# Optimization experiments

Measured on AMD Instinct MI355X. Metric: run time of the kernel, lower is better.

The kernel has to match this reference:

```python
import math
import jax, jax.numpy as jnp
import numpy as np

WINDOW_SHAPE = [30, 30, 8]
DEPTH = 8
NUM_DIMS = 3
N_POINTS = 2_000_000
BATCH = 4
SPARSE_SHAPE = np.array([32, 512, 512], dtype=np.int64)  # [D, H, W]


def _right_shift_bits(b, k):
    # shift bit-array right along last axis: prepend k zeros, drop last k
    if b.shape[-1] <= k:
        return jnp.zeros_like(b)
    pad = [(0, 0)] * (b.ndim - 1) + [(k, 0)]
    return jnp.pad(b[..., :-k], pad)


def _gray2binary(gray):
    # prefix-XOR along last axis via doubling (matches torch gray2binary)
    n = gray.shape[-1]
    shift = 2 ** (math.ceil(math.log2(n)) - 1)
    while shift > 0:
        gray = jnp.logical_xor(gray, _right_shift_bits(gray, shift))
        shift //= 2
    return gray


def hilbert_encode(locs, num_dims, num_bits):
    # locs: [N, num_dims] int, each in [0, 2**num_bits)
    n = locs.shape[0]
    # bit b of gray is the (num_bits-1-b)-th bit of the coordinate (MSB first)
    shifts_ = (num_bits - 1 - jnp.arange(num_bits, dtype=locs.dtype))
    gray = ((locs[:, :, None] >> shifts_[None, None, :]) & 1).astype(bool)  # [N, D, B]
    # Skilling's transform: small fixed loop (num_bits*num_dims = 24 iters)
    for bit in range(num_bits):
        for dim in range(num_dims):
            mask = gray[:, dim, bit]  # [N]
            g0 = jnp.logical_xor(gray[:, 0, bit + 1:], mask[:, None])
            gray = gray.at[:, 0, bit + 1:].set(g0)
            to_flip = jnp.logical_and(
                jnp.logical_not(mask)[:, None],
                jnp.logical_xor(gray[:, 0, bit + 1:], gray[:, dim, bit + 1:]),
            )
            gray = gray.at[:, dim, bit + 1:].set(
                jnp.logical_xor(gray[:, dim, bit + 1:], to_flip))
            gray = gray.at[:, 0, bit + 1:].set(
                jnp.logical_xor(gray[:, 0, bit + 1:], to_flip))
    # interleave: swapaxes(1,2) then flatten -> [N, num_bits*num_dims], MSB first
    bits = jnp.transpose(gray, (0, 2, 1)).reshape(n, num_bits * num_dims)
    hb = _gray2binary(bits)
    nb = num_bits * num_dims
    weights = jnp.asarray((1 << (nb - 1 - np.arange(nb))), dtype=jnp.int32)
    code = (hb.astype(jnp.int32) * weights).sum(-1)
    return code


def setup_inputs() -> dict:
    key = jax.random.key(0)
    kb, kz, ky, kx = jax.random.split(key, 4)
    D, H, W = [int(v) for v in SPARSE_SHAPE]
    b = jax.random.randint(kb, (N_POINTS,), 0, BATCH, dtype=jnp.int32)
    z = jax.random.randint(kz, (N_POINTS,), 0, D, dtype=jnp.int32)
    y = jax.random.randint(ky, (N_POINTS,), 0, H, dtype=jnp.int32)
    x = jax.random.randint(kx, (N_POINTS,), 0, W, dtype=jnp.int32)
    coords = jnp.stack([b, z, y, x], axis=-1)  # [N, 4]: bs, z, y, x
    return {"coords": coords, "sparse_shape": SPARSE_SHAPE, "shifts": 1}


def reference(coords, sparse_shape, shifts):
    # sparse_shape is static config: [D, H, W]; reversed -> W, H, D (as in torch)
    ss = [int(v) for v in np.asarray(sparse_shape)][::-1]
    W, H, D = ss
    wx, wy, wz = WINDOW_SHAPE
    if bool(shifts):
        sx, sy, sz = math.ceil(wx / 2), math.ceil(wy / 2), math.ceil(wz / 2)
    else:
        sx = sy = sz = 0
    b = coords[:, 0]
    x = (coords[:, 3] + sx) % W
    y = (coords[:, 2] + sy) % H
    z = (coords[:, 1] + sz) % D
    locs = jnp.stack([x, y, z], axis=-1)  # [N, 3]
    code = hilbert_encode(locs, NUM_DIMS, DEPTH)
    code = code | (b.astype(code.dtype) << (DEPTH * 3))
    coords2curve = jnp.argsort(code)
    return coords2curve
```

## Files before the change

### kernel.cpp

```cpp
#include <hip/hip_runtime.h>
#include <stdint.h>


#define THREADS 512
#define TILE 4096
#define ROUNDS (TILE / THREADS)
#define WAVES (THREADS / 64)
#define CHUNK (TILE / WAVES)
#define IDX_BITS 22
#define IDX_MASK 0x3FFFFFu

__device__ __forceinline__ int tile_of(int bid, int nwg) {
  int q = nwg >> 3, r = nwg & 7;
  int x = bid & 7, k = bid >> 3;
  return x * q + (x < r ? x : r) + k;
}

__device__ __forceinline__ uint32_t hilbert_code(uint32_t x, uint32_t y, uint32_t z) {
  uint32_t X0 = x & 255u, X1 = y & 255u, X2 = z & 255u;
#pragma unroll
  for (int p = 7; p >= 0; --p) {
    uint32_t low = (1u << p) - 1u;
    uint32_t f0 = (uint32_t)-(int)((X0 >> p) & 1u);
    X0 ^= (low & f0);
    uint32_t f1 = (uint32_t)-(int)((X1 >> p) & 1u);
    uint32_t t1 = ((X0 ^ X1) & low) & ~f1;
    X0 ^= (low & f1) ^ t1;
    X1 ^= t1;
    uint32_t f2 = (uint32_t)-(int)((X2 >> p) & 1u);
    uint32_t t2 = ((X0 ^ X2) & low) & ~f2;
    X0 ^= (low & f2) ^ t2;
    X2 ^= t2;
  }
  uint32_t G = 0;
#pragma unroll
  for (int k = 0; k < 8; ++k) {
    int p = 7 - k;
    G |= ((X0 >> p) & 1u) << (23 - 3 * k);
    G |= ((X1 >> p) & 1u) << (22 - 3 * k);
    G |= ((X2 >> p) & 1u) << (21 - 3 * k);
  }
  G ^= G >> 16; G ^= G >> 8; G ^= G >> 4; G ^= G >> 2; G ^= G >> 1;
  return G & 0xFFFFFFu;
}

__global__ __launch_bounds__(THREADS) void genkeys_hist(
    const int4* __restrict__ coords, const void* __restrict__ ss,
    const int* __restrict__ shifts, uint32_t* __restrict__ keys0,
    int* __restrict__ hist, int N) {
  __shared__ int lh[512];
  int t = threadIdx.x, b = tile_of(blockIdx.x, gridDim.x);
  lh[t] = 0;

  const int* p32 = (const int*)ss;
  int D, H, W;
  if (p32[1] == 0) { const long long* p64 = (const long long*)ss;
    D = (int)p64[0]; H = (int)p64[1]; W = (int)p64[2]; }
  else { D = p32[0]; H = p32[1]; W = p32[2]; }
  int sflag = shifts[0];
  int sx = sflag ? 15 : 0, sy = sflag ? 15 : 0, sz = sflag ? 4 : 0;
  bool wp2 = (W & (W - 1)) == 0, hp2 = (H & (H - 1)) == 0, dp2 = (D & (D - 1)) == 0;
  __syncthreads();

#pragma unroll
  for (int r = 0; r < ROUNDS; ++r) {
    int idx = b * TILE + r * THREADS + t;
    if (idx < N) {
      int4 c = coords[idx];
      uint32_t bb = (uint32_t)c.x;
      int zz = c.y + sz, yy = c.z + sy, xx = c.w + sx;
      uint32_t z = (uint32_t)(dp2 ? (zz & (D - 1)) : (zz % D));
      uint32_t y = (uint32_t)(hp2 ? (yy & (H - 1)) : (yy % H));
      uint32_t x = (uint32_t)(wp2 ? (xx & (W - 1)) : (xx % W));
      uint32_t code = hilbert_code(x, y, z) | (bb << 24);
      keys0[idx] = code;
      atomicAdd(&lh[code & 511u], 1);
    }
  }
  __syncthreads();
  hist[(size_t)b * 512 + t] = lh[t];
}

template <int SHIFT, int NB>
__global__ __launch_bounds__(THREADS) void hist_kernel(
    const uint32_t* __restrict__ keys, int* __restrict__ hist, int N) {
  __shared__ int lh[NB];
  int t = threadIdx.x, b = tile_of(blockIdx.x, gridDim.x);
  if (t < NB) lh[t] = 0;
  __syncthreads();
#pragma unroll
  for (int r = 0; r < ROUNDS; ++r) {
    int idx = b * TILE + r * THREADS + t;
    if (idx < N) atomicAdd(&lh[(keys[idx] >> SHIFT) & (NB - 1)], 1);
  }
  __syncthreads();
  if (t < NB) hist[(size_t)b * NB + t] = lh[t];
}

__global__ __launch_bounds__(512) void scan_blocks(
    int* __restrict__ hist, int* __restrict__ digitTotals, int nblocks, int nbins) {
  __shared__ int wsum[8];
  int d = blockIdx.x, t = threadIdx.x, wave = t >> 6, lane = t & 63;
  int carry = 0;
  for (int start = 0; start < nblocks; start += 512) {
    int i = start + t;
    int vv = (i < nblocks) ? hist[(size_t)i * nbins + d] : 0;
    int x = vv;
#pragma unroll
    for (int off = 1; off < 64; off <<= 1) {
      int n = __shfl_up(x, off);
      if (lane >= off) x += n;
    }
    if (lane == 63) wsum[wave] = x;
    __syncthreads();
    int pre = 0;
    for (int w = 0; w < wave; ++w) pre += wsum[w];
    if (i < nblocks) hist[(size_t)i * nbins + d] = carry + pre + x - vv;
    int tot = 0;
    for (int w = 0; w < 8; ++w) tot += wsum[w];
    __syncthreads();
    carry += tot;
  }
  if (t == 0) digitTotals[d] = carry;
}

template <int MODE>
__global__ __launch_bounds__(THREADS) void scatter_kernel(
    const uint32_t* __restrict__ in0, const uint32_t* __restrict__ in1,
    uint32_t* __restrict__ out0, uint32_t* __restrict__ out1,
    const int* __restrict__ hist, const int* __restrict__ digitTotals, int N) {
  constexpr int NB = (MODE == 2) ? 256 : 512;
  constexpr int RB = (MODE == 2) ? 8 : 9;
  constexpr int SHIFT = (MODE == 0) ? 0 : (MODE == 1) ? 9 : 22;
  __shared__ uint64_t sbuf[(MODE == 2) ? TILE / 2 : TILE];
  __shared__ __align__(16) unsigned short cnt[WAVES][NB];
  int t = threadIdx.x, b = tile_of(blockIdx.x, gridDim.x);
  int wave = t >> 6, lane = t & 63;

  int histv = 0, dt = 0;
  if (t < NB) {
    histv = hist[(size_t)b * NB + t];
    dt = digitTotals[t];
  }
  for (int i = t; i < WAVES * NB; i += THREADS) ((unsigned short*)cnt)[i] = 0;
  __syncthreads();

  uint64_t kvR[ROUNDS];
  int drR[ROUNDS];
  uint64_t ltm = (1ull << lane) - 1ull;
  int chunk0 = b * TILE + wave * CHUNK;

#pragma unroll
  for (int r = 0; r < ROUNDS; ++r) {
    int idx = chunk0 + r * 64 + lane;
    bool valid = idx < N;
    uint32_t a = valid ? in0[idx] : 0u;
    uint64_t kv;
    if (MODE == 0)      kv = ((uint64_t)(uint32_t)idx << 32) | a;
    else if (MODE == 1) kv = ((uint64_t)(valid ? in1[idx] : 0u) << 32) | a;
    else                kv = a;
    kvR[r] = kv;
    int digit = (int)((a >> SHIFT) & (NB - 1));
    uint64_t eq = __ballot(valid);
#pragma unroll
    for (int bit = 0; bit < RB; ++bit) {
      uint64_t m = __ballot((digit >> bit) & 1);
      eq &= ((digit >> bit) & 1) ? m : ~m;
    }
    int waveRank = __popcll(eq & ltm);
    int cntW = __popcll(eq);
    int prior = cnt[wave][digit];
    drR[r] = valid ? (digit | ((prior + waveRank) << RB)) : -1;
    if (valid && waveRank == 0) cnt[wave][digit] = (unsigned short)(prior + cntW);
  }
  __syncthreads();

  int2* wt = (int2*)sbuf;
  int tot = 0, adjv = 0;
  int2 v = make_int2(0, 0);
  if (t < NB) {
#pragma unroll
    for (int w = 0; w < WAVES; ++w) tot += cnt[w][t];
    v = make_int2(tot, dt);
#pragma unroll
    for (int off = 1; off < 64; off <<= 1) {
      int nx = __shfl_up(v.x, off), ny = __shfl_up(v.y, off);
      if (lane >= off) { v.x += nx; v.y += ny; }
    }
    if (lane == 63) wt[wave] = v;
  }
  __syncthreads();
  if (t < NB) {
    int2 pre = make_int2(0, 0);
    for (int w = 0; w < wave; ++w) { pre.x += wt[w].x; pre.y += wt[w].y; }
    int ds = pre.x + v.x - tot;
    adjv = histv + (pre.y + v.y - dt) - ds;
    int run = ds;
#pragma unroll
    for (int w = 0; w < WAVES; ++w) {
      int x = cnt[w][t];
      cnt[w][t] = (unsigned short)run;
      run += x;
    }
  }
  __syncthreads();

#pragma unroll
  for (int r = 0; r < ROUNDS; ++r) {
    int dr = drR[r];
    if (dr >= 0) {
      int digit = dr & (NB - 1);
      int rnk = dr >> RB;
      int slot = (int)cnt[wave][digit] + rnk;
      if (MODE == 2) ((uint32_t*)sbuf)[slot] = (uint32_t)kvR[r];
      else           sbuf[slot] = kvR[r];
    }
  }
  __syncthreads();

  int* adjArr = (int*)cnt;
  if (t < NB) adjArr[t] = adjv;
  __syncthreads();

  int validCount = min(TILE, N - b * TILE);
#pragma unroll
  for (int j = 0; j < ROUNDS; ++j) {
    int i = j * THREADS + t;
    if (i < validCount) {
      if (MODE == 0) {
        uint64_t kv = sbuf[i];
        uint32_t key = (uint32_t)kv;
        int pos = adjArr[key & 511u] + i;
        out0[pos] = key;
        out1[pos] = (uint32_t)(kv >> 32);
      } else if (MODE == 1) {
        uint64_t kv = sbuf[i];
        uint32_t key = (uint32_t)kv, idxv = (uint32_t)(kv >> 32);
        int pos = adjArr[(key >> 9) & 511u] + i;
        out0[pos] = ((key >> 18) << IDX_BITS) | idxv;
      } else {
        uint32_t p = ((uint32_t*)sbuf)[i];
        int pos = adjArr[(p >> IDX_BITS) & 255u] + i;
        out0[pos] = p & IDX_MASK;
      }
    }
  }
}

extern "C" void kernel_launch(void* const* d_in, const int* in_sizes, int n_in,
                              void* d_out, int out_size, void* d_ws, size_t ws_size,
                              hipStream_t stream) {
  const int4* coords = (const int4*)d_in[0];
  const void* ss = d_in[1];
  const int* shifts = (const int*)d_in[2];
  int N = in_sizes[0] / 4;
  int nblocks = (N + TILE - 1) / TILE;

  char* ws = (char*)d_ws;
  size_t off = 0;
  auto alloc = [&](size_t bytes) -> void* {
    void* p = ws + off;
    off += (bytes + 255) & ~(size_t)255;
    return p;
  };
  uint32_t* keys0 = (uint32_t*)alloc((size_t)N * 4);
  uint32_t* keys1 = (uint32_t*)alloc((size_t)N * 4);
  uint32_t* vals1 = (uint32_t*)alloc((size_t)N * 4);
  uint32_t* packd = (uint32_t*)alloc((size_t)N * 4);
  int*      hist  = (int*)alloc((size_t)512 * nblocks * 4);
  int*      digitTotals = (int*)alloc(512 * 4);

  genkeys_hist<<<nblocks, THREADS, 0, stream>>>(coords, ss, shifts, keys0, hist, N);
  scan_blocks<<<512, 512, 0, stream>>>(hist, digitTotals, nblocks, 512);
  scatter_kernel<0><<<nblocks, THREADS, 0, stream>>>(
      keys0, nullptr, keys1, vals1, hist, digitTotals, N);

  hist_kernel<9, 512><<<nblocks, THREADS, 0, stream>>>(keys1, hist, N);
  scan_blocks<<<512, 512, 0, stream>>>(hist, digitTotals, nblocks, 512);
  scatter_kernel<1><<<nblocks, THREADS, 0, stream>>>(
      keys1, vals1, packd, nullptr, hist, digitTotals, N);

  hist_kernel<22, 256><<<nblocks, THREADS, 0, stream>>>(packd, hist, N);
  scan_blocks<<<256, 512, 0, stream>>>(hist, digitTotals, nblocks, 256);
  scatter_kernel<2><<<nblocks, THREADS, 0, stream>>>(
      packd, nullptr, (uint32_t*)d_out, nullptr, hist, digitTotals, N);
}
```

Measured before the change: 82.60 us.

## Fuse next-pass histograms into radix scatter and double last-pass tile size

Removes the two standalone histogram kernels. Each scatter pass now accumulates the next pass's per-tile digit histogram with global atomics, keyed by output position. This saves a full read of the keys per pass and two launches, at the cost of up to one global atomic per element and a memset of the histogram buffers. The final 8-bit pass now uses 8192-element tiles, halving its block count and doubling per-thread register and LDS footprint.

```diff
diff --git a/kernel.cpp b/kernel.cpp
--- a/kernel.cpp
+++ b/kernel.cpp
@@ -4,9 +4,9 @@
 
 #define THREADS 512
 #define TILE 4096
+#define TILE2 8192
 #define ROUNDS (TILE / THREADS)
 #define WAVES (THREADS / 64)
-#define CHUNK (TILE / WAVES)
 #define IDX_BITS 22
 #define IDX_MASK 0x3FFFFFu
 
@@ -81,22 +81,6 @@
   hist[(size_t)b * 512 + t] = lh[t];
 }
 
-template <int SHIFT, int NB>
-__global__ __launch_bounds__(THREADS) void hist_kernel(
-    const uint32_t* __restrict__ keys, int* __restrict__ hist, int N) {
-  __shared__ int lh[NB];
-  int t = threadIdx.x, b = tile_of(blockIdx.x, gridDim.x);
-  if (t < NB) lh[t] = 0;
-  __syncthreads();
-#pragma unroll
-  for (int r = 0; r < ROUNDS; ++r) {
-    int idx = b * TILE + r * THREADS + t;
-    if (idx < N) atomicAdd(&lh[(keys[idx] >> SHIFT) & (NB - 1)], 1);
-  }
-  __syncthreads();
-  if (t < NB) hist[(size_t)b * NB + t] = lh[t];
-}
-
 __global__ __launch_bounds__(512) void scan_blocks(
     int* __restrict__ hist, int* __restrict__ digitTotals, int nblocks, int nbins) {
   __shared__ int wsum[8];
@@ -128,11 +112,15 @@
 __global__ __launch_bounds__(THREADS) void scatter_kernel(
     const uint32_t* __restrict__ in0, const uint32_t* __restrict__ in1,
     uint32_t* __restrict__ out0, uint32_t* __restrict__ out1,
-    const int* __restrict__ hist, const int* __restrict__ digitTotals, int N) {
+    const int* __restrict__ hist, const int* __restrict__ digitTotals,
+    int* __restrict__ histNext, int N) {
   constexpr int NB = (MODE == 2) ? 256 : 512;
   constexpr int RB = (MODE == 2) ? 8 : 9;
   constexpr int SHIFT = (MODE == 0) ? 0 : (MODE == 1) ? 9 : 22;
-  __shared__ uint64_t sbuf[(MODE == 2) ? TILE / 2 : TILE];
+  constexpr int TB = (MODE == 2) ? TILE2 : TILE;
+  constexpr int RNDS = TB / THREADS;
+  constexpr int CH = TB / WAVES;
+  __shared__ uint64_t sbuf[(MODE == 2) ? TILE2 / 2 : TILE];
   __shared__ __align__(16) unsigned short cnt[WAVES][NB];
   int t = threadIdx.x, b = tile_of(blockIdx.x, gridDim.x);
   int wave = t >> 6, lane = t & 63;
@@ -145,13 +133,13 @@
   for (int i = t; i < WAVES * NB; i += THREADS) ((unsigned short*)cnt)[i] = 0;
   __syncthreads();
 
-  uint64_t kvR[ROUNDS];
-  int drR[ROUNDS];
+  uint64_t kvR[RNDS];
+  int drR[RNDS];
   uint64_t ltm = (1ull << lane) - 1ull;
-  int chunk0 = b * TILE + wave * CHUNK;
-
-#pragma unroll
-  for (int r = 0; r < ROUNDS; ++r) {
+  int chunk0 = b * TB + wave * CH;
+
+#pragma unroll
+  for (int r = 0; r < RNDS; ++r) {
     int idx = chunk0 + r * 64 + lane;
     bool valid = idx < N;
     uint32_t a = valid ? in0[idx] : 0u;
@@ -206,7 +194,7 @@
   __syncthreads();
 
 #pragma unroll
-  for (int r = 0; r < ROUNDS; ++r) {
+  for (int r = 0; r < RNDS; ++r) {
     int dr = drR[r];
     if (dr >= 0) {
       int digit = dr & (NB - 1);
@@ -222,9 +210,9 @@
   if (t < NB) adjArr[t] = adjv;
   __syncthreads();
 
-  int validCount = min(TILE, N - b * TILE);
-#pragma unroll
-  for (int j = 0; j < ROUNDS; ++j) {
+  int validCount = min(TB, N - b * TB);
+#pragma unroll
+  for (int j = 0; j < RNDS; ++j) {
     int i = j * THREADS + t;
     if (i < validCount) {
       if (MODE == 0) {
@@ -233,11 +221,13 @@
         int pos = adjArr[key & 511u] + i;
         out0[pos] = key;
         out1[pos] = (uint32_t)(kv >> 32);
+        atomicAdd(&histNext[(size_t)(pos >> 12) * 512 + ((key >> 9) & 511u)], 1);
       } else if (MODE == 1) {
         uint64_t kv = sbuf[i];
         uint32_t key = (uint32_t)kv, idxv = (uint32_t)(kv >> 32);
         int pos = adjArr[(key >> 9) & 511u] + i;
         out0[pos] = ((key >> 18) << IDX_BITS) | idxv;
+        atomicAdd(&histNext[(size_t)(pos >> 13) * 256 + ((key >> 18) & 255u)], 1);
       } else {
         uint32_t p = ((uint32_t*)sbuf)[i];
         int pos = adjArr[(p >> IDX_BITS) & 255u] + i;
@@ -255,6 +245,7 @@
   const int* shifts = (const int*)d_in[2];
   int N = in_sizes[0] / 4;
   int nblocks = (N + TILE - 1) / TILE;
+  int nblocks2 = (N + TILE2 - 1) / TILE2;
 
   char* ws = (char*)d_ws;
   size_t off = 0;
@@ -267,21 +258,24 @@
   uint32_t* keys1 = (uint32_t*)alloc((size_t)N * 4);
   uint32_t* vals1 = (uint32_t*)alloc((size_t)N * 4);
   uint32_t* packd = (uint32_t*)alloc((size_t)N * 4);
-  int*      hist  = (int*)alloc((size_t)512 * nblocks * 4);
+  int*      histA = (int*)alloc((size_t)512 * nblocks * 4);
+  int*      histB = (int*)alloc((size_t)512 * nblocks * 4);
+  int*      histC = (int*)alloc((size_t)256 * nblocks2 * 4);
   int*      digitTotals = (int*)alloc(512 * 4);
 
-  genkeys_hist<<<nblocks, THREADS, 0, stream>>>(coords, ss, shifts, keys0, hist, N);
-  scan_blocks<<<512, 512, 0, stream>>>(hist, digitTotals, nblocks, 512);
+  size_t zbytes = (size_t)((char*)histC - (char*)histB) + (size_t)256 * nblocks2 * 4;
+  hipMemsetAsync(histB, 0, zbytes, stream);
+
+  genkeys_hist<<<nblocks, THREADS, 0, stream>>>(coords, ss, shifts, keys0, histA, N);
+  scan_blocks<<<512, 512, 0, stream>>>(histA, digitTotals, nblocks, 512);
   scatter_kernel<0><<<nblocks, THREADS, 0, stream>>>(
-      keys0, nullptr, keys1, vals1, hist, digitTotals, N);
-
-  hist_kernel<9, 512><<<nblocks, THREADS, 0, stream>>>(keys1, hist, N);
-  scan_blocks<<<512, 512, 0, stream>>>(hist, digitTotals, nblocks, 512);
+      keys0, nullptr, keys1, vals1, histA, digitTotals, histB, N);
+
+  scan_blocks<<<512, 512, 0, stream>>>(histB, digitTotals, nblocks, 512);
   scatter_kernel<1><<<nblocks, THREADS, 0, stream>>>(
-      keys1, vals1, packd, nullptr, hist, digitTotals, N);
-
-  hist_kernel<22, 256><<<nblocks, THREADS, 0, stream>>>(packd, hist, N);
-  scan_blocks<<<256, 512, 0, stream>>>(hist, digitTotals, nblocks, 256);
-  scatter_kernel<2><<<nblocks, THREADS, 0, stream>>>(
-      packd, nullptr, (uint32_t*)d_out, nullptr, hist, digitTotals, N);
-}
+      keys1, vals1, packd, nullptr, histB, digitTotals, histC, N);
+
+  scan_blocks<<<256, 512, 0, stream>>>(histC, digitTotals, nblocks2, 256);
+  scatter_kernel<2><<<nblocks2, THREADS, 0, stream>>>(
+      packd, nullptr, (uint32_t*)d_out, nullptr, histC, digitTotals, nullptr, N);
+}
```

Result: slower. 233.3 us (+182.4%).

## Use larger tiles for final radix pass and vectorize histogram loads

Applied to the files above, without the earlier changes.

The final 8-bit radix pass now works on 8192-element tiles instead of 4096, which halves the block count and the per-block histogram and scan work for that pass. The histogram kernel reads four keys at a time with uint4 loads. The scatter kernel keeps keys and values as separate 32-bit registers and builds the index payload only at the LDS write, which lowers register pressure for the larger tile. In exchange, the final scatter holds more register state per thread and gets fewer blocks per CU, which can reduce occupancy.

```diff
diff --git a/kernel.cpp b/kernel.cpp
--- a/kernel.cpp
+++ b/kernel.cpp
@@ -4,9 +4,8 @@
 
 #define THREADS 512
 #define TILE 4096
-#define ROUNDS (TILE / THREADS)
+#define TILE2 8192
 #define WAVES (THREADS / 64)
-#define CHUNK (TILE / WAVES)
 #define IDX_BITS 22
 #define IDX_MASK 0x3FFFFFu
 
@@ -63,7 +62,7 @@
   __syncthreads();
 
 #pragma unroll
-  for (int r = 0; r < ROUNDS; ++r) {
+  for (int r = 0; r < TILE / THREADS; ++r) {
     int idx = b * TILE + r * THREADS + t;
     if (idx < N) {
       int4 c = coords[idx];
@@ -81,7 +80,7 @@
   hist[(size_t)b * 512 + t] = lh[t];
 }
 
-template <int SHIFT, int NB>
+template <int SHIFT, int NB, int TB>
 __global__ __launch_bounds__(THREADS) void hist_kernel(
     const uint32_t* __restrict__ keys, int* __restrict__ hist, int N) {
   __shared__ int lh[NB];
@@ -89,9 +88,18 @@
   if (t < NB) lh[t] = 0;
   __syncthreads();
 #pragma unroll
-  for (int r = 0; r < ROUNDS; ++r) {
-    int idx = b * TILE + r * THREADS + t;
-    if (idx < N) atomicAdd(&lh[(keys[idx] >> SHIFT) & (NB - 1)], 1);
+  for (int r = 0; r < TB / THREADS / 4; ++r) {
+    int base = b * TB + (r * THREADS + t) * 4;
+    if (base + 3 < N) {
+      uint4 k = *(const uint4*)(keys + base);
+      atomicAdd(&lh[(k.x >> SHIFT) & (NB - 1)], 1);
+      atomicAdd(&lh[(k.y >> SHIFT) & (NB - 1)], 1);
+      atomicAdd(&lh[(k.z >> SHIFT) & (NB - 1)], 1);
+      atomicAdd(&lh[(k.w >> SHIFT) & (NB - 1)], 1);
+    } else {
+      for (int u = 0; u < 4; ++u)
+        if (base + u < N) atomicAdd(&lh[(keys[base + u] >> SHIFT) & (NB - 1)], 1);
+    }
   }
   __syncthreads();
   if (t < NB) hist[(size_t)b * NB + t] = lh[t];
@@ -132,7 +140,10 @@
   constexpr int NB = (MODE == 2) ? 256 : 512;
   constexpr int RB = (MODE == 2) ? 8 : 9;
   constexpr int SHIFT = (MODE == 0) ? 0 : (MODE == 1) ? 9 : 22;
-  __shared__ uint64_t sbuf[(MODE == 2) ? TILE / 2 : TILE];
+  constexpr int TB = (MODE == 2) ? TILE2 : TILE;
+  constexpr int RNDS = TB / THREADS;
+  constexpr int CH = TB / WAVES;
+  __shared__ uint64_t sbuf[TB <= 4096 ? TB : TB / 2];
   __shared__ __align__(16) unsigned short cnt[WAVES][NB];
   int t = threadIdx.x, b = tile_of(blockIdx.x, gridDim.x);
   int wave = t >> 6, lane = t & 63;
@@ -145,21 +156,19 @@
   for (int i = t; i < WAVES * NB; i += THREADS) ((unsigned short*)cnt)[i] = 0;
   __syncthreads();
 
-  uint64_t kvR[ROUNDS];
-  int drR[ROUNDS];
+  uint32_t kR[RNDS];
+  uint32_t vR[(MODE == 1) ? RNDS : 1];
+  int drR[RNDS];
   uint64_t ltm = (1ull << lane) - 1ull;
-  int chunk0 = b * TILE + wave * CHUNK;
-
-#pragma unroll
-  for (int r = 0; r < ROUNDS; ++r) {
+  int chunk0 = b * TB + wave * CH;
+
+#pragma unroll
+  for (int r = 0; r < RNDS; ++r) {
     int idx = chunk0 + r * 64 + lane;
     bool valid = idx < N;
     uint32_t a = valid ? in0[idx] : 0u;
-    uint64_t kv;
-    if (MODE == 0)      kv = ((uint64_t)(uint32_t)idx << 32) | a;
-    else if (MODE == 1) kv = ((uint64_t)(valid ? in1[idx] : 0u) << 32) | a;
-    else                kv = a;
-    kvR[r] = kv;
+    kR[r] = a;
+    if (MODE == 1) vR[r] = valid ? in1[idx] : 0u;
     int digit = (int)((a >> SHIFT) & (NB - 1));
     uint64_t eq = __ballot(valid);
 #pragma unroll
@@ -206,14 +215,20 @@
   __syncthreads();
 
 #pragma unroll
-  for (int r = 0; r < ROUNDS; ++r) {
+  for (int r = 0; r < RNDS; ++r) {
     int dr = drR[r];
     if (dr >= 0) {
       int digit = dr & (NB - 1);
       int rnk = dr >> RB;
       int slot = (int)cnt[wave][digit] + rnk;
-      if (MODE == 2) ((uint32_t*)sbuf)[slot] = (uint32_t)kvR[r];
-      else           sbuf[slot] = kvR[r];
+      if (MODE == 0) {
+        uint32_t idxv = (uint32_t)(chunk0 + r * 64 + lane);
+        sbuf[slot] = ((uint64_t)idxv << 32) | kR[r];
+      } else if (MODE == 1) {
+        sbuf[slot] = ((uint64_t)vR[r] << 32) | kR[r];
+      } else {
+        ((uint32_t*)sbuf)[slot] = kR[r];
+      }
     }
   }
   __syncthreads();
@@ -222,9 +237,9 @@
   if (t < NB) adjArr[t] = adjv;
   __syncthreads();
 
-  int validCount = min(TILE, N - b * TILE);
-#pragma unroll
-  for (int j = 0; j < ROUNDS; ++j) {
+  int validCount = min(TB, N - b * TB);
+#pragma unroll
+  for (int j = 0; j < RNDS; ++j) {
     int i = j * THREADS + t;
     if (i < validCount) {
       if (MODE == 0) {
@@ -255,6 +270,7 @@
   const int* shifts = (const int*)d_in[2];
   int N = in_sizes[0] / 4;
   int nblocks = (N + TILE - 1) / TILE;
+  int nblocks2 = (N + TILE2 - 1) / TILE2;
 
   char* ws = (char*)d_ws;
   size_t off = 0;
@@ -275,13 +291,13 @@
   scatter_kernel<0><<<nblocks, THREADS, 0, stream>>>(
       keys0, nullptr, keys1, vals1, hist, digitTotals, N);
 
-  hist_kernel<9, 512><<<nblocks, THREADS, 0, stream>>>(keys1, hist, N);
+  hist_kernel<9, 512, TILE><<<nblocks, THREADS, 0, stream>>>(keys1, hist, N);
   scan_blocks<<<512, 512, 0, stream>>>(hist, digitTotals, nblocks, 512);
   scatter_kernel<1><<<nblocks, THREADS, 0, stream>>>(
       keys1, vals1, packd, nullptr, hist, digitTotals, N);
 
-  hist_kernel<22, 256><<<nblocks, THREADS, 0, stream>>>(packd, hist, N);
-  scan_blocks<<<256, 512, 0, stream>>>(hist, digitTotals, nblocks, 256);
-  scatter_kernel<2><<<nblocks, THREADS, 0, stream>>>(
+  hist_kernel<22, 256, TILE2><<<nblocks2, THREADS, 0, stream>>>(packd, hist, N);
+  scan_blocks<<<256, 512, 0, stream>>>(hist, digitTotals, nblocks2, 256);
+  scatter_kernel<2><<<nblocks2, THREADS, 0, stream>>>(
       packd, nullptr, (uint32_t*)d_out, nullptr, hist, digitTotals, N);
 }
```

Result: no change. 83.27 us (+0.8%).
